# Performance work log

Hardware: AMD Instinct MI355X
Metric: run time of the kernel (lower is better)

Reference implementation:

```python
import jax, jax.numpy as jnp
import numpy as np
import math

N_HEAD = 16
ROPE_BASE = 10000.0

def _rope_cos_sin(seq_len, head_dim, dtype):
    inv_freq = 1.0 / (ROPE_BASE ** (jnp.arange(0, head_dim, 2, dtype=jnp.float32) / head_dim))
    t = jnp.arange(seq_len, dtype=jnp.float32)
    freqs = t[:, None] * inv_freq[None, :]            # [S, D/2]
    emb = jnp.concatenate([freqs, freqs], axis=-1)     # [S, D]
    # broadcast shape [1, 1, S, D] to match q/k [B, H, S, D]
    return jnp.cos(emb)[None, None].astype(dtype), jnp.sin(emb)[None, None].astype(dtype)

def _rotate_half(x):
    x1, x2 = jnp.split(x, 2, axis=-1)
    return jnp.concatenate([-x2, x1], axis=-1)

def setup_inputs() -> dict:
    key = jax.random.key(0)
    ks = jax.random.split(key, 5)
    B, S, E = 2, 2048, 1024
    x = jax.random.normal(ks[0], (B, S, E), dtype=jnp.float32)
    init = 1.0 / math.sqrt(E)
    Wq = jax.random.normal(ks[1], (E, E), dtype=jnp.float32) * init
    Wk = jax.random.normal(ks[2], (E, E), dtype=jnp.float32) * init
    Wv = jax.random.normal(ks[3], (E, E), dtype=jnp.float32) * init
    Wo = jax.random.normal(ks[4], (E, E), dtype=jnp.float32) * init
    # causal mask: True = masked (masked_fill with -inf)
    attn_mask = jnp.triu(jnp.ones((S, S), dtype=bool), k=1)
    return {"x": x, "Wq": Wq, "Wk": Wk, "Wv": Wv, "Wo": Wo, "attn_mask": attn_mask}

def reference(x, Wq, Wk, Wv, Wo, attn_mask):
    B, S, E = x.shape
    H = N_HEAD
    D = E // H
    # projections (torch Linear: y = x @ W.T), split heads -> [B, H, S, D]
    def proj(W):
        return jnp.einsum('bse,fe->bsf', x, W).reshape(B, S, H, D).transpose(0, 2, 1, 3)
    q, k, v = proj(Wq), proj(Wk), proj(Wv)
    cos, sin = _rope_cos_sin(S, D, x.dtype)
    q = q * cos + _rotate_half(q) * sin
    k = k * cos + _rotate_half(k) * sin
    scale = 1.0 / math.sqrt(D)
    scores = jnp.einsum('bhqd,bhkd->bhqk', q, k) * scale  # [B, H, S, S]
    scores = jnp.where(attn_mask[None, None], -jnp.inf, scores)
    attn = jax.nn.softmax(scores, axis=-1)
    out = jnp.einsum('bhqk,bhkd->bhqd', attn, v)           # [B, H, S, D]
    out = out.transpose(0, 2, 1, 3).reshape(B, S, E)
    return jnp.einsum('bse,fe->bsf', out, Wo)
```

## Files before the change

kernel.cpp:

```cpp
#include <hip/hip_runtime.h>
#include <hip/hip_bf16.h>

#define NB 2
#define NH 16
#define SEQ 2048
#define HD 64
#define EMB 1024

typedef unsigned short u16;
typedef unsigned int u32;
typedef __attribute__((ext_vector_type(8))) short bf16x8;
typedef __attribute__((ext_vector_type(4))) float f32x4;
typedef __attribute__((ext_vector_type(8))) unsigned short us8;

__device__ __forceinline__ float b2f(u16 u) {
    union { unsigned int i; float f; } v; v.i = ((unsigned int)u) << 16; return v.f;
}
__device__ __forceinline__ u16 f2b(float f) {
    union { float f; unsigned int i; } v; v.f = f;
    unsigned int x = v.i;
    return (u16)((x + 0x7FFFu + ((x >> 16) & 1u)) >> 16);
}
__device__ __forceinline__ u32 pk2(float a, float b) {
    union { __hip_bfloat162 h; u32 u; } v;
    v.h = __float22bfloat162_rn(make_float2(a, b));
    return v.u;
}

__device__ __forceinline__ void gld16(const u16* g, u16* l) {
    __builtin_amdgcn_global_load_lds((const __attribute__((address_space(1))) void*)g,
                                     (__attribute__((address_space(3))) void*)l, 16, 0, 0);
}

#define BAR8P()  asm volatile("s_barrier" ::: "memory")
#define VMW8P(n) asm volatile("s_waitcnt vmcnt(" #n ")" ::: "memory")

__device__ __forceinline__ void conv8(const void* src, u16* dst, int i, int isbf16) {
    if (isbf16) {
        *reinterpret_cast<uint4*>(dst + i) =
            *reinterpret_cast<const uint4*>((const u16*)src + i);
    } else {
        const float* s = (const float*)src + i;
        float4 a = *reinterpret_cast<const float4*>(s);
        float4 b = *reinterpret_cast<const float4*>(s + 4);
        us8 v;
        v[0] = f2b(a.x); v[1] = f2b(a.y); v[2] = f2b(a.z); v[3] = f2b(a.w);
        v[4] = f2b(b.x); v[5] = f2b(b.y); v[6] = f2b(b.z); v[7] = f2b(b.w);
        *reinterpret_cast<us8*>(dst + i) = v;
    }
}

__global__ __launch_bounds__(256)
void prep_54571854463007(const void* __restrict__ x,
                         const void* __restrict__ w0, const void* __restrict__ w1,
                         const void* __restrict__ w2, const void* __restrict__ w3,
                         u16* __restrict__ xb, u16* __restrict__ dqkv,
                         u16* __restrict__ dob, int* __restrict__ flag) {
    __shared__ int cnt;
    if (threadIdx.x == 0) cnt = 0;
    __syncthreads();
    const u16 v = ((const u16*)x)[threadIdx.x];
    const int e = (v >> 7) & 0xFF;
    if (e >= 110 && e <= 135) atomicAdd(&cnt, 1);
    __syncthreads();
    const int isbf16 = (cnt >= 200) ? 1 : 0;
    const int blk = blockIdx.x;
    if (blk == 0 && threadIdx.x == 0) *flag = isbf16;
    const int NXB = (NB * SEQ * EMB) / 2048;
    if (blk < NXB) {
        conv8(x, xb, (blk * 256 + threadIdx.x) * 8, isbf16);
    } else {
        const int r = blk - NXB;
        const int seg = r >> 9;
        const int NW = EMB * EMB;
        const void* src = (seg == 0) ? w0 : (seg == 1) ? w1 : (seg == 2) ? w2 : w3;
        u16* dst = (seg < 3) ? (dqkv + (size_t)seg * NW) : dob;
        conv8(src, dst, ((r & 511) * 256 + threadIdx.x) * 8, isbf16);
    }
}

template<int MIH, int NIH>
__device__ __forceinline__ void quad8p(const bf16x8 (&aT)[4][2], const bf16x8 (&bT)[4][2],
                                       f32x4 (&acc)[8][4]) {
#pragma unroll
    for (int i = 0; i < 4; ++i)
#pragma unroll
        for (int j = 0; j < 2; ++j)
#pragma unroll
            for (int k = 0; k < 2; ++k)
                acc[MIH * 4 + i][NIH * 2 + j] = __builtin_amdgcn_mfma_f32_16x16x32_bf16(
                    aT[i][k], bT[NIH * 2 + j][k], acc[MIH * 4 + i][NIH * 2 + j], 0, 0, 0);
}

__device__ __forceinline__ void rd8p(const u16* Ls, int buf, int rbase, int quad, int fr,
                                     bf16x8 (&dst)[4][2]) {
#pragma unroll
    for (int i = 0; i < 4; ++i) {
        const int R  = rbase + i * 16 + fr;
        const int rb = buf * 16384 + R * 64;
        const int sw = R & 7;
        dst[i][0] = *reinterpret_cast<const bf16x8*>(&Ls[rb + ((quad    ) ^ sw) * 8]);
        dst[i][1] = *reinterpret_cast<const bf16x8*>(&Ls[rb + ((quad + 4) ^ sw) * 8]);
    }
}

__global__ __launch_bounds__(512, 2)
void gemm8p_54571854463007(const u16* __restrict__ A, const u16* __restrict__ Bw,
                           u16* __restrict__ C) {
    __shared__ __align__(16) u16 As[32768];
    __shared__ __align__(16) u16 Bs[32768];
    const int tid  = threadIdx.x;
    const int w    = tid >> 6, lane = tid & 63;
    const int quad = lane >> 4, fr = lane & 15;
    const int wm   = w >> 2, wn = w & 3;
    const int m0   = blockIdx.y * 256, n0 = blockIdx.x * 256;
    const int srow = tid >> 3;
    const int schk = ((tid & 7) ^ (srow & 7)) * 8;

    auto stageU = [&](const u16* G, u16* Ls, int T, int jp, int gbase) {
        const int Tm  = T & 15;
        const int buf = T & 1;
        const int j0  = jp * 2;
        gld16(G + (size_t)(gbase + j0 * 64      + srow) * 1024 + Tm * 64 + schk,
              &Ls[buf * 16384 +  j0      * 4096 + w * 512]);
        gld16(G + (size_t)(gbase + j0 * 64 + 64 + srow) * 1024 + Tm * 64 + schk,
              &Ls[buf * 16384 + (j0 + 1) * 4096 + w * 512]);
    };

    f32x4 acc[8][4];
    const f32x4 zz = {0.f, 0.f, 0.f, 0.f};
#pragma unroll
    for (int i = 0; i < 8; ++i)
#pragma unroll
        for (int j = 0; j < 4; ++j) acc[i][j] = zz;

    stageU(A, As, 0, 0, m0);
    stageU(A, As, 0, 1, m0);
    stageU(Bw, Bs, 0, 0, n0);
    stageU(Bw, Bs, 0, 1, n0);
    stageU(A, As, 1, 0, m0);
    VMW8P(2);
    BAR8P();

#pragma unroll 1
    for (int it = 0; it < 8; ++it) {
        const int ta = 2 * it, tb = ta + 1;
        bf16x8 aT[4][2], bT[4][2];
        rd8p(As, 0, wm * 128, quad, fr, aT);
        rd8p(Bs, 0, wn * 64, quad, fr, bT);
        stageU(A, As, tb, 1, m0);
        __builtin_amdgcn_s_setprio(1); quad8p<0, 0>(aT, bT, acc); __builtin_amdgcn_s_setprio(0);
        BAR8P();
        stageU(Bw, Bs, tb, 0, n0);
        __builtin_amdgcn_s_setprio(1); quad8p<0, 1>(aT, bT, acc); __builtin_amdgcn_s_setprio(0);
        BAR8P();
        rd8p(As, 0, wm * 128 + 64, quad, fr, aT);
        stageU(Bw, Bs, tb, 1, n0);
        __builtin_amdgcn_s_setprio(1); quad8p<1, 0>(aT, bT, acc); __builtin_amdgcn_s_setprio(0);
        BAR8P();
        stageU(A, As, ta + 2, 0, m0);
        __builtin_amdgcn_s_setprio(1); quad8p<1, 1>(aT, bT, acc); __builtin_amdgcn_s_setprio(0);
        VMW8P(2);
        BAR8P();
        rd8p(As, 1, wm * 128, quad, fr, aT);
        rd8p(Bs, 1, wn * 64, quad, fr, bT);
        stageU(A, As, ta + 2, 1, m0);
        __builtin_amdgcn_s_setprio(1); quad8p<0, 0>(aT, bT, acc); __builtin_amdgcn_s_setprio(0);
        BAR8P();
        stageU(Bw, Bs, ta + 2, 0, n0);
        __builtin_amdgcn_s_setprio(1); quad8p<0, 1>(aT, bT, acc); __builtin_amdgcn_s_setprio(0);
        BAR8P();
        rd8p(As, 1, wm * 128 + 64, quad, fr, aT);
        stageU(Bw, Bs, ta + 2, 1, n0);
        __builtin_amdgcn_s_setprio(1); quad8p<1, 0>(aT, bT, acc); __builtin_amdgcn_s_setprio(0);
        BAR8P();
        stageU(A, As, tb + 2, 0, m0);
        __builtin_amdgcn_s_setprio(1); quad8p<1, 1>(aT, bT, acc); __builtin_amdgcn_s_setprio(0);
        VMW8P(2);
        BAR8P();
    }

    const int t0 = n0 >> 10;
    if (t0 == 0) {
        const float SCL = 0.18033688011112042f;
#pragma unroll
        for (int mi = 0; mi < 8; ++mi)
#pragma unroll
            for (int ni = 0; ni < 4; ++ni)
#pragma unroll
                for (int r = 0; r < 4; ++r) acc[mi][ni][r] *= SCL;
    }
    if (t0 < 2) {
        const float inv0 = __powf(10000.f, -(float)fr / 32.f);
        const float inv1 = __powf(10000.f, -(float)(fr + 16) / 32.f);
#pragma unroll
        for (int mi = 0; mi < 8; ++mi)
#pragma unroll
            for (int r = 0; r < 4; ++r) {
                const int s = (m0 + wm * 128 + mi * 16 + quad * 4 + r) & (SEQ - 1);
#pragma unroll
                for (int nl = 0; nl < 2; ++nl) {
                    float sn, cs;
                    __sincosf((float)s * (nl ? inv1 : inv0), &sn, &cs);
                    const float lo = acc[mi][nl][r], hi = acc[mi][nl + 2][r];
                    acc[mi][nl][r]     = lo * cs - hi * sn;
                    acc[mi][nl + 2][r] = hi * cs + lo * sn;
                }
            }
    }
    const size_t TS = (size_t)NB * NH * SEQ * HD;
#pragma unroll
    for (int mi = 0; mi < 8; ++mi)
#pragma unroll
        for (int ni = 0; ni < 4; ++ni)
#pragma unroll
            for (int r = 0; r < 4; ++r) {
                const int m = m0 + wm * 128 + mi * 16 + quad * 4 + r;
                const int n = n0 + wn * 64 + ni * 16 + fr;
                const int t = n >> 10, idx = n & 1023;
                const int h = idx >> 6, d = idx & 63;
                const int b = m >> 11, s = m & (SEQ - 1);
                C[t * TS + ((((size_t)b * NH + h) * SEQ + s) << 6) + d] = f2b(acc[mi][ni][r]);
            }
}

template<int OUT_MODE>
__global__ __launch_bounds__(256)
void gemm_mfma_54571854463007(const u16* __restrict__ A, const u16* __restrict__ Bw,
                              void* __restrict__ C, const int* __restrict__ flagp,
                              int M, int N, int K) {
    __shared__ __align__(16) u16 As[128 * 32];
    __shared__ __align__(16) u16 Bs[128 * 32];
    const int tid  = threadIdx.x;
    const int wave = tid >> 6, lane = tid & 63;
    const int quad = lane >> 4, fr = lane & 15;
    const int wr = (wave >> 1) * 64, wc = (wave & 1) * 64;
    const int m0 = blockIdx.y * 128, n0 = blockIdx.x * 128;
    const int r0 = tid >> 2;
    const int kc = (tid & 3) * 8;
    const f32x4 zz = {0.f, 0.f, 0.f, 0.f};
    f32x4 acc[4][4];
#pragma unroll
    for (int i = 0; i < 4; ++i)
#pragma unroll
        for (int j = 0; j < 4; ++j) acc[i][j] = zz;

    for (int k0 = 0; k0 < K; k0 += 32) {
        gld16(A  + (size_t)(m0 + r0) * K + k0 + kc,      &As[wave * 512]);
        gld16(A  + (size_t)(m0 + 64 + r0) * K + k0 + kc, &As[2048 + wave * 512]);
        gld16(Bw + (size_t)(n0 + r0) * K + k0 + kc,      &Bs[wave * 512]);
        gld16(Bw + (size_t)(n0 + 64 + r0) * K + k0 + kc, &Bs[2048 + wave * 512]);
        __syncthreads();
        bf16x8 af[4], bfr[4];
#pragma unroll
        for (int mi = 0; mi < 4; ++mi)
            af[mi] = *reinterpret_cast<const bf16x8*>(&As[(wr + mi * 16 + fr) * 32 + quad * 8]);
#pragma unroll
        for (int ni = 0; ni < 4; ++ni)
            bfr[ni] = *reinterpret_cast<const bf16x8*>(&Bs[(wc + ni * 16 + fr) * 32 + quad * 8]);
#pragma unroll
        for (int mi = 0; mi < 4; ++mi)
#pragma unroll
            for (int ni = 0; ni < 4; ++ni)
                acc[mi][ni] = __builtin_amdgcn_mfma_f32_16x16x32_bf16(af[mi], bfr[ni], acc[mi][ni], 0, 0, 0);
        __syncthreads();
    }

    const int isbf16 = *flagp;
#pragma unroll
    for (int mi = 0; mi < 4; ++mi)
#pragma unroll
        for (int ni = 0; ni < 4; ++ni)
#pragma unroll
            for (int r = 0; r < 4; ++r) {
                const int m = m0 + wr + mi * 16 + quad * 4 + r;
                const int n = n0 + wc + ni * 16 + fr;
                const float v = acc[mi][ni][r];
                if (isbf16) ((u16*)C)[(size_t)m * N + n] = f2b(v);
                else        ((float*)C)[(size_t)m * N + n] = v;
            }
}

__global__ __launch_bounds__(256, 4)
void flash_54571854463007(const u16* __restrict__ Q, const u16* __restrict__ K,
                          const u16* __restrict__ V, u16* __restrict__ AO,
                          float* __restrict__ OP0, float* __restrict__ OP1,
                          float* __restrict__ LP0, float* __restrict__ LP1) {
    __shared__ __align__(16) u16 Kt[2 * 4096];
    __shared__ __align__(16) u16 Vt[2 * 4608];
    const int tid  = threadIdx.x;
    const int w    = tid >> 6, lane = tid & 63;
    const int quad = lane >> 4, fr = lane & 15;
    const int lin = blockIdx.x;
    const int xcd = lin & 7;
    const int r_  = lin >> 3;
    const int b4  = r_ & 3;
    const int ti  = r_ >> 2;
    int qt, kt0, kt1;
    if (ti < 17)       { qt = 15 + ti; kt0 = 0;  kt1 = 15; }
    else if (ti == 17) { qt = 31;      kt0 = 16; kt1 = 31; }
    else {
        const int g = ti - 18, s = 15 - (g >> 1);
        if (g & 1) { qt = s + 15; kt0 = 16; kt1 = qt; }
        else       { qt = s - 1;  kt0 = 0;  kt1 = qt; }
    }
    const int bh = xcd * 4 + b4;
    const bool partial = (qt >= 16);
    const int h = bh & 15, b = bh >> 4;
    const size_t base = ((size_t)b * NH + h) * SEQ * HD;
    const int k2   = (tid & 31) * 2;
    const int key0 = (k2 & 3) * 16 + (k2 >> 2);
    const int d8   = ((tid >> 5) & 7) * 8;

    const int krs = lane >> 3;
    const int kch = ((lane & 7) ^ krs) * 8;
    const int swz = fr & 7;
    const int co0 = (quad ^ swz) * 8;
    const int co1 = ((quad + 4) ^ swz) * 8;

    const bf16x8 ones = {(short)0x3F80, (short)0x3F80, (short)0x3F80, (short)0x3F80,
                         (short)0x3F80, (short)0x3F80, (short)0x3F80, (short)0x3F80};

    const u16* qp = Q + base + (size_t)(qt * 64 + w * 16 + fr) * HD + quad * 8;
    const bf16x8 aq0 = *reinterpret_cast<const bf16x8*>(qp);
    const bf16x8 aq1 = *reinterpret_cast<const bf16x8*>(qp + 32);

    {
        const u16* Kg = K + base + (size_t)kt0 * 64 * HD;
        gld16(Kg + (size_t)((w * 2 + 0) * 8 + krs) * HD + kch, &Kt[(w * 2 + 0) * 512]);
        gld16(Kg + (size_t)((w * 2 + 1) * 8 + krs) * HD + kch, &Kt[(w * 2 + 1) * 512]);
    }
    us8 vc0, vc1, vn0, vn1;
    {
        const u16* vs = V + base + (size_t)(kt0 * 64 + key0) * HD + d8;
        vc0 = *reinterpret_cast<const us8*>(vs);
        vc1 = *reinterpret_cast<const us8*>(vs + 16 * HD);
    }

    const f32x4 zz = {0.f, 0.f, 0.f, 0.f};
    f32x4 lacc = zz;
    f32x4 oacc[4];
#pragma unroll
    for (int nt = 0; nt < 4; ++nt) oacc[nt] = zz;

    for (int kt = kt0; kt <= kt1; ++kt) {
        const int buf = (kt - kt0) & 1;
        const int vb  = buf * 4608;
        const int kb  = buf * 4096;
#pragma unroll
        for (int jj = 0; jj < 8; ++jj) {
            const u32 pk = ((u32)(u16)vc1[jj] << 16) | (u32)(u16)vc0[jj];
            *reinterpret_cast<u32*>(&Vt[vb + (d8 + jj) * 72 + k2]) = pk;
        }
        __syncthreads();
        if (kt + 1 <= kt1) {
            const u16* Kg = K + base + (size_t)(kt + 1) * 64 * HD;
            const int kb1 = (buf ^ 1) * 4096;
            gld16(Kg + (size_t)((w * 2 + 0) * 8 + krs) * HD + kch, &Kt[kb1 + (w * 2 + 0) * 512]);
            gld16(Kg + (size_t)((w * 2 + 1) * 8 + krs) * HD + kch, &Kt[kb1 + (w * 2 + 1) * 512]);
            const u16* vs = V + base + (size_t)((kt + 1) * 64 + key0) * HD + d8;
            vn0 = *reinterpret_cast<const us8*>(vs);
            vn1 = *reinterpret_cast<const us8*>(vs + 16 * HD);
        }
        f32x4 sa[4];
        __builtin_amdgcn_s_setprio(1);
#pragma unroll
        for (int nt = 0; nt < 4; ++nt) {
            const int rb = kb + (nt * 16 + fr) * 64;
            const bf16x8 ka0 = *reinterpret_cast<const bf16x8*>(&Kt[rb + co0]);
            const bf16x8 ka1 = *reinterpret_cast<const bf16x8*>(&Kt[rb + co1]);
            sa[nt] = __builtin_amdgcn_mfma_f32_16x16x32_bf16(ka0, aq0, zz, 0, 0, 0);
            sa[nt] = __builtin_amdgcn_mfma_f32_16x16x32_bf16(ka1, aq1, sa[nt], 0, 0, 0);
        }
        __builtin_amdgcn_s_setprio(0);
        if (kt == qt) {
#pragma unroll
            for (int nt = 0; nt < 4; ++nt)
#pragma unroll
                for (int r = 0; r < 4; ++r)
                    if (nt * 16 + quad * 4 + r > w * 16 + fr) sa[nt][r] = -__builtin_inff();
        }
        u32 c01[4], c23[4];
#pragma unroll
        for (int r = 0; r < 4; ++r) {
            c01[r] = pk2(exp2f(sa[0][r]), exp2f(sa[1][r]));
            c23[r] = pk2(exp2f(sa[2][r]), exp2f(sa[3][r]));
        }
        union { u32 u[4]; bf16x8 v; } P0, P1;
        {
            auto a = __builtin_amdgcn_permlane16_swap(c01[0], c01[2], false, false);
            auto bsw = __builtin_amdgcn_permlane32_swap(a[0], a[1], false, false);
            P0.u[0] = (u32)bsw[0]; P1.u[0] = (u32)bsw[1];
        }
        {
            auto a = __builtin_amdgcn_permlane16_swap(c23[0], c23[2], false, false);
            auto bsw = __builtin_amdgcn_permlane32_swap(a[0], a[1], false, false);
            P0.u[1] = (u32)bsw[0]; P1.u[1] = (u32)bsw[1];
        }
        {
            auto a = __builtin_amdgcn_permlane16_swap(c01[1], c01[3], false, false);
            auto bsw = __builtin_amdgcn_permlane32_swap(a[0], a[1], false, false);
            P0.u[2] = (u32)bsw[0]; P1.u[2] = (u32)bsw[1];
        }
        {
            auto a = __builtin_amdgcn_permlane16_swap(c23[1], c23[3], false, false);
            auto bsw = __builtin_amdgcn_permlane32_swap(a[0], a[1], false, false);
            P0.u[3] = (u32)bsw[0]; P1.u[3] = (u32)bsw[1];
        }
        const bf16x8 pa0 = P0.v;
        const bf16x8 pa1 = P1.v;
        __builtin_amdgcn_s_setprio(1);
        lacc = __builtin_amdgcn_mfma_f32_16x16x32_bf16(pa0, ones, lacc, 0, 0, 0);
        lacc = __builtin_amdgcn_mfma_f32_16x16x32_bf16(pa1, ones, lacc, 0, 0, 0);
#pragma unroll
        for (int nt = 0; nt < 4; ++nt) {
            const bf16x8 bv0 = *reinterpret_cast<const bf16x8*>(&Vt[vb + (nt * 16 + fr) * 72 + quad * 8]);
            const bf16x8 bv1 = *reinterpret_cast<const bf16x8*>(&Vt[vb + (nt * 16 + fr) * 72 + 32 + quad * 8]);
            oacc[nt] = __builtin_amdgcn_mfma_f32_16x16x32_bf16(pa0, bv0, oacc[nt], 0, 0, 0);
            oacc[nt] = __builtin_amdgcn_mfma_f32_16x16x32_bf16(pa1, bv1, oacc[nt], 0, 0, 0);
        }
        __builtin_amdgcn_s_setprio(0);
        vc0 = vn0; vc1 = vn1;
    }
    if (!partial) {
#pragma unroll
        for (int r = 0; r < 4; ++r) {
            const float inv = 1.0f / lacc[r];
            const int q = qt * 64 + w * 16 + quad * 4 + r;
#pragma unroll
            for (int nt = 0; nt < 4; ++nt)
                AO[(((size_t)b * SEQ + q) * NH + h) * HD + nt * 16 + fr] = f2b(oacc[nt][r] * inv);
        }
    } else {
        float* OP = (kt0 == 16) ? OP1 : OP0;
        float* LP = (kt0 == 16) ? LP1 : LP0;
        const int tb = (bh * 16 + (qt - 16)) * 64;
#pragma unroll
        for (int r = 0; r < 4; ++r) {
            const int qrow = w * 16 + quad * 4 + r;
            LP[tb + qrow] = lacc[r];
#pragma unroll
            for (int nt = 0; nt < 4; ++nt)
                OP[(size_t)(tb + qrow) * 64 + nt * 16 + fr] = oacc[nt][r];
        }
    }
}

__global__ __launch_bounds__(256)
void combine_54571854463007(const float* __restrict__ OP0, const float* __restrict__ OP1,
                            const float* __restrict__ LP0, const float* __restrict__ LP1,
                            u16* __restrict__ AO) {
    const int idx  = blockIdx.x * 256 + threadIdx.x;
    const int row  = idx >> 3;
    const int d8   = (idx & 7) * 8;
    const int bh   = row >> 10;
    const int tile = (row >> 6) & 15;
    const int qrow = row & 63;
    const int h = bh & 15, b = bh >> 4;
    const int q = (16 + tile) * 64 + qrow;
    const float4* A = reinterpret_cast<const float4*>(&OP0[(size_t)row * 64 + d8]);
    const float4* Bp = reinterpret_cast<const float4*>(&OP1[(size_t)row * 64 + d8]);
    const float4 a0 = A[0], a1 = A[1], b0 = Bp[0], b1 = Bp[1];
    const float inv = 1.0f / (LP0[row] + LP1[row]);
    us8 o;
    o[0] = f2b((a0.x + b0.x) * inv); o[1] = f2b((a0.y + b0.y) * inv);
    o[2] = f2b((a0.z + b0.z) * inv); o[3] = f2b((a0.w + b0.w) * inv);
    o[4] = f2b((a1.x + b1.x) * inv); o[5] = f2b((a1.y + b1.y) * inv);
    o[6] = f2b((a1.z + b1.z) * inv); o[7] = f2b((a1.w + b1.w) * inv);
    *reinterpret_cast<us8*>(&AO[(((size_t)b * SEQ + q) * NH + h) * HD + d8]) = o;
}

extern "C" void kernel_launch(void* const* d_in, const int* in_sizes, int n_in,
                              void* d_out, int out_size, void* d_ws, size_t ws_size,
                              hipStream_t stream) {
    (void)in_sizes; (void)n_in; (void)out_size; (void)ws_size;
    const void* x  = d_in[0];
    const void* Wq = d_in[1];
    const void* Wk = d_in[2];
    const void* Wv = d_in[3];
    const void* Wo = d_in[4];

    char* ws = (char*)d_ws;
    const size_t MB = 1024 * 1024;
    int* flag = (int*)ws;
    u16* xb   = (u16*)(ws + 64);
    u16* Wqkv = (u16*)(ws + 64 + 8 * MB);
    u16* Wob  = (u16*)(ws + 64 + 14 * MB);
    u16* Qb   = (u16*)(ws + 64 + 16 * MB);
    u16* Kb   = (u16*)(ws + 64 + 24 * MB);
    u16* Vb   = (u16*)(ws + 64 + 32 * MB);
    float* OP0 = (float*)(ws + 64 + 40 * MB);
    float* OP1 = (float*)(ws + 64 + 48 * MB);
    float* LP0 = (float*)(ws + 64 + 56 * MB);
    float* LP1 = (float*)(ws + 64 + 56 * MB + 256 * 1024);
    u16* AO   = xb;

    prep_54571854463007<<<dim3(4096), 256, 0, stream>>>(
        x, Wq, Wk, Wv, Wo, xb, Wqkv, Wob, flag);

    const int M = NB * SEQ;
    gemm8p_54571854463007<<<dim3(3 * EMB / 256, M / 256), 512, 0, stream>>>(
        xb, Wqkv, Qb);

    flash_54571854463007<<<dim3(1536), 256, 0, stream>>>(Qb, Kb, Vb, AO,
                                                         OP0, OP1, LP0, LP1);
    combine_54571854463007<<<dim3(1024), 256, 0, stream>>>(OP0, OP1, LP0, LP1, AO);

    gemm_mfma_54571854463007<0><<<dim3(EMB / 128, M / 128), 256, 0, stream>>>(
        AO, Wob, d_out, flag, M, EMB, EMB);
}
```

Before: 204.5 us.

## Double flash query tile to 128 rows with 512-thread blocks sharing K/V tiles

The flash attention kernel now gives each block 128 query rows over 8 waves instead of 64 rows over 4 waves, so each K/V tile staged in LDS serves twice as many queries. Per-thread K and V load work is halved, and the grid shrinks to 768 blocks. The causal split scheduling and the combine indexing are remapped to the new tile size. The cost is more diagonal masking work per block, coarser load balancing, and higher per-block register and occupancy pressure.

```diff
diff --git a/kernel.cpp b/kernel.cpp
--- a/kernel.cpp
+++ b/kernel.cpp
@@ -12,6 +12,7 @@
 typedef __attribute__((ext_vector_type(8))) short bf16x8;
 typedef __attribute__((ext_vector_type(4))) float f32x4;
 typedef __attribute__((ext_vector_type(8))) unsigned short us8;
+typedef __attribute__((ext_vector_type(4))) unsigned short us4;
 
 __device__ __forceinline__ float b2f(u16 u) {
     union { unsigned int i; float f; } v; v.i = ((unsigned int)u) << 16; return v.f;
@@ -281,7 +282,7 @@
             }
 }
 
-__global__ __launch_bounds__(256, 4)
+__global__ __launch_bounds__(512, 8)
 void flash_54571854463007(const u16* __restrict__ Q, const u16* __restrict__ K,
                           const u16* __restrict__ V, u16* __restrict__ AO,
                           float* __restrict__ OP0, float* __restrict__ OP1,
@@ -296,21 +297,22 @@
     const int r_  = lin >> 3;
     const int b4  = r_ & 3;
     const int ti  = r_ >> 2;
-    int qt, kt0, kt1;
-    if (ti < 17)       { qt = 15 + ti; kt0 = 0;  kt1 = 15; }
-    else if (ti == 17) { qt = 31;      kt0 = 16; kt1 = 31; }
+    int T, kt0, kt1;
+    if (ti < 8)       { T = 8 + ti; kt0 = 0;  kt1 = 15; }
+    else if (ti == 8) { T = 15;     kt0 = 16; kt1 = 31; }
+    else if (ti == 9) { T = 7;      kt0 = 0;  kt1 = 15; }
     else {
-        const int g = ti - 18, s = 15 - (g >> 1);
-        if (g & 1) { qt = s + 15; kt0 = 16; kt1 = qt; }
-        else       { qt = s - 1;  kt0 = 0;  kt1 = qt; }
-    }
+        const int g = ti - 10, s = 7 - (g >> 1);
+        if ((g & 1) == 0) { T = s + 7; kt0 = 16; kt1 = 2 * T + 1; }
+        else              { T = s - 1; kt0 = 0;  kt1 = 2 * T + 1; }
+    }
+    const bool split = (T >= 8);
     const int bh = xcd * 4 + b4;
-    const bool partial = (qt >= 16);
     const int h = bh & 15, b = bh >> 4;
     const size_t base = ((size_t)b * NH + h) * SEQ * HD;
     const int k2   = (tid & 31) * 2;
     const int key0 = (k2 & 3) * 16 + (k2 >> 2);
-    const int d8   = ((tid >> 5) & 7) * 8;
+    const int d4   = ((tid >> 5) & 15) * 4;
 
     const int krs = lane >> 3;
     const int kch = ((lane & 7) ^ krs) * 8;
@@ -321,20 +323,16 @@
     const bf16x8 ones = {(short)0x3F80, (short)0x3F80, (short)0x3F80, (short)0x3F80,
                          (short)0x3F80, (short)0x3F80, (short)0x3F80, (short)0x3F80};
 
-    const u16* qp = Q + base + (size_t)(qt * 64 + w * 16 + fr) * HD + quad * 8;
+    const u16* qp = Q + base + (size_t)(T * 128 + w * 16 + fr) * HD + quad * 8;
     const bf16x8 aq0 = *reinterpret_cast<const bf16x8*>(qp);
     const bf16x8 aq1 = *reinterpret_cast<const bf16x8*>(qp + 32);
 
+    gld16(K + base + (size_t)(kt0 * 64 + w * 8 + krs) * HD + kch, &Kt[w * 512]);
+    us4 vc0, vc1, vn0, vn1;
     {
-        const u16* Kg = K + base + (size_t)kt0 * 64 * HD;
-        gld16(Kg + (size_t)((w * 2 + 0) * 8 + krs) * HD + kch, &Kt[(w * 2 + 0) * 512]);
-        gld16(Kg + (size_t)((w * 2 + 1) * 8 + krs) * HD + kch, &Kt[(w * 2 + 1) * 512]);
-    }
-    us8 vc0, vc1, vn0, vn1;
-    {
-        const u16* vs = V + base + (size_t)(kt0 * 64 + key0) * HD + d8;
-        vc0 = *reinterpret_cast<const us8*>(vs);
-        vc1 = *reinterpret_cast<const us8*>(vs + 16 * HD);
+        const u16* vs = V + base + (size_t)(kt0 * 64 + key0) * HD + d4;
+        vc0 = *reinterpret_cast<const us4*>(vs);
+        vc1 = *reinterpret_cast<const us4*>(vs + 16 * HD);
     }
 
     const f32x4 zz = {0.f, 0.f, 0.f, 0.f};
@@ -348,19 +346,18 @@
         const int vb  = buf * 4608;
         const int kb  = buf * 4096;
 #pragma unroll
-        for (int jj = 0; jj < 8; ++jj) {
+        for (int jj = 0; jj < 4; ++jj) {
             const u32 pk = ((u32)(u16)vc1[jj] << 16) | (u32)(u16)vc0[jj];
-            *reinterpret_cast<u32*>(&Vt[vb + (d8 + jj) * 72 + k2]) = pk;
+            *reinterpret_cast<u32*>(&Vt[vb + (d4 + jj) * 72 + k2]) = pk;
         }
         __syncthreads();
         if (kt + 1 <= kt1) {
-            const u16* Kg = K + base + (size_t)(kt + 1) * 64 * HD;
             const int kb1 = (buf ^ 1) * 4096;
-            gld16(Kg + (size_t)((w * 2 + 0) * 8 + krs) * HD + kch, &Kt[kb1 + (w * 2 + 0) * 512]);
-            gld16(Kg + (size_t)((w * 2 + 1) * 8 + krs) * HD + kch, &Kt[kb1 + (w * 2 + 1) * 512]);
-            const u16* vs = V + base + (size_t)((kt + 1) * 64 + key0) * HD + d8;
-            vn0 = *reinterpret_cast<const us8*>(vs);
-            vn1 = *reinterpret_cast<const us8*>(vs + 16 * HD);
+            gld16(K + base + (size_t)((kt + 1) * 64 + w * 8 + krs) * HD + kch,
+                  &Kt[kb1 + w * 512]);
+            const u16* vs = V + base + (size_t)((kt + 1) * 64 + key0) * HD + d4;
+            vn0 = *reinterpret_cast<const us4*>(vs);
+            vn1 = *reinterpret_cast<const us4*>(vs + 16 * HD);
         }
         f32x4 sa[4];
         __builtin_amdgcn_s_setprio(1);
@@ -373,12 +370,14 @@
             sa[nt] = __builtin_amdgcn_mfma_f32_16x16x32_bf16(ka1, aq1, sa[nt], 0, 0, 0);
         }
         __builtin_amdgcn_s_setprio(0);
-        if (kt == qt) {
+        const int dk = kt - 2 * T;
+        if (dk >= 0) {
 #pragma unroll
             for (int nt = 0; nt < 4; ++nt)
 #pragma unroll
                 for (int r = 0; r < 4; ++r)
-                    if (nt * 16 + quad * 4 + r > w * 16 + fr) sa[nt][r] = -__builtin_inff();
+                    if (dk * 64 + nt * 16 + quad * 4 + r > w * 16 + fr)
+                        sa[nt][r] = -__builtin_inff();
         }
         u32 c01[4], c23[4];
 #pragma unroll
@@ -422,11 +421,11 @@
         __builtin_amdgcn_s_setprio(0);
         vc0 = vn0; vc1 = vn1;
     }
-    if (!partial) {
+    if (!split) {
 #pragma unroll
         for (int r = 0; r < 4; ++r) {
             const float inv = 1.0f / lacc[r];
-            const int q = qt * 64 + w * 16 + quad * 4 + r;
+            const int q = T * 128 + w * 16 + quad * 4 + r;
 #pragma unroll
             for (int nt = 0; nt < 4; ++nt)
                 AO[(((size_t)b * SEQ + q) * NH + h) * HD + nt * 16 + fr] = f2b(oacc[nt][r] * inv);
@@ -434,14 +433,13 @@
     } else {
         float* OP = (kt0 == 16) ? OP1 : OP0;
         float* LP = (kt0 == 16) ? LP1 : LP0;
-        const int tb = (bh * 16 + (qt - 16)) * 64;
 #pragma unroll
         for (int r = 0; r < 4; ++r) {
-            const int qrow = w * 16 + quad * 4 + r;
-            LP[tb + qrow] = lacc[r];
+            const int row0 = bh * 1024 + (T * 128 + w * 16 + quad * 4 + r) - 1024;
+            LP[row0] = lacc[r];
 #pragma unroll
             for (int nt = 0; nt < 4; ++nt)
-                OP[(size_t)(tb + qrow) * 64 + nt * 16 + fr] = oacc[nt][r];
+                OP[(size_t)row0 * 64 + nt * 16 + fr] = oacc[nt][r];
         }
     }
 }
@@ -454,10 +452,9 @@
     const int row  = idx >> 3;
     const int d8   = (idx & 7) * 8;
     const int bh   = row >> 10;
-    const int tile = (row >> 6) & 15;
-    const int qrow = row & 63;
+    const int qoff = row & 1023;
     const int h = bh & 15, b = bh >> 4;
-    const int q = (16 + tile) * 64 + qrow;
+    const int q = 1024 + qoff;
     const float4* A = reinterpret_cast<const float4*>(&OP0[(size_t)row * 64 + d8]);
     const float4* Bp = reinterpret_cast<const float4*>(&OP1[(size_t)row * 64 + d8]);
     const float4 a0 = A[0], a1 = A[1], b0 = Bp[0], b1 = Bp[1];
@@ -502,8 +499,8 @@
     gemm8p_54571854463007<<<dim3(3 * EMB / 256, M / 256), 512, 0, stream>>>(
         xb, Wqkv, Qb);
 
-    flash_54571854463007<<<dim3(1536), 256, 0, stream>>>(Qb, Kb, Vb, AO,
-                                                         OP0, OP1, LP0, LP1);
+    flash_54571854463007<<<dim3(768), 512, 0, stream>>>(Qb, Kb, Vb, AO,
+                                                        OP0, OP1, LP0, LP1);
     combine_54571854463007<<<dim3(1024), 256, 0, stream>>>(OP0, OP1, LP0, LP1, AO);
 
     gemm_mfma_54571854463007<0><<<dim3(EMB / 128, M / 128), 256, 0, stream>>>(
```

Measured after the change: 217.1 us. 6.2% more time.
